# Kernel tuning notes

Hardware: AMD Instinct MI355X
Metric: run time of the kernel (lower is better)

The kernel has to match this reference:

```python
import jax, jax.numpy as jnp
import numpy as np

N = 50000      # number of graph nodes
D = 128        # in_dim == out_dim
R = 4          # num_ring
NNZ = 800000   # edges per ring (avg degree 16)


def setup_inputs() -> dict:
    key = jax.random.key(0)
    ks = jax.random.split(key, 12)
    s = 1.0 / np.sqrt(D)
    x = jax.random.normal(ks[0], (N, D), jnp.float32)
    W_self = jax.random.normal(ks[1], (D, D), jnp.float32) * s
    W_rings = jax.random.normal(ks[2], (R, D, D), jnp.float32) * s
    WC = jax.random.normal(ks[3], (D, D), jnp.float32) * s
    WD = jax.random.normal(ks[4], (D, D), jnp.float32) * s
    att_w = jax.random.normal(ks[5], (1, 2 * (R + 1) * D), jnp.float32) * s
    att_b = jnp.zeros((1,), jnp.float32)
    # degree^-0.5 style norms: positive, in (0, 1]
    out_deg_norm = jax.random.uniform(ks[6], (N, 1), jnp.float32, 0.05, 1.0)
    in_deg_norm = jax.random.uniform(ks[7], (N, 1), jnp.float32, 0.05, 1.0)
    rows = jax.random.randint(ks[8], (R, NNZ), 0, N, jnp.int32)
    cols = jax.random.randint(ks[9], (R, NNZ), 0, N, jnp.int32)
    return {"x": x, "W_self": W_self, "W_rings": W_rings, "WC": WC, "WD": WD,
            "att_w": att_w, "att_b": att_b, "out_deg_norm": out_deg_norm,
            "in_deg_norm": in_deg_norm, "rows": rows, "cols": cols}


def reference(x, W_self, W_rings, WC, WD, att_w, att_b, out_deg_norm, in_deg_norm, rows, cols):
    n, d = x.shape
    r = W_rings.shape[0]
    # ---- ring-wise sparse aggregation (dropout is identity at inference) ----
    z_self = x @ W_self.T                       # [N, D]
    z_list = [z_self]
    for i in range(r):
        h = (x @ W_rings[i].T) * out_deg_norm   # [N, D]
        # torch.sparse.mm(adj, h): out[row] += h[col] for each edge (row, col)
        z_i = jax.ops.segment_sum(h[cols[i]], rows[i], num_segments=n)
        z_list.append(z_i)
    z = jnp.concatenate(z_list, axis=1) * in_deg_norm   # [N, (R+1)*D]
    # ---- heterogeneous sensitivity interaction ----
    z3 = z.reshape(n, r + 1, d)                          # [N, R+1, D]
    z_hat_com = z3 @ WC                                  # [N, R+1, D]
    com_score = jnp.einsum('nrd,nsd->nrs', z_hat_com, z_hat_com)
    alpha_com = jax.nn.softmax(com_score, axis=-1)
    z_com = jnp.einsum('nrs,nsd->nrd', alpha_com, z_hat_com).reshape(n, -1)
    z_hat_dis = z3 @ WD                                  # [N, R+1, D]
    # pairwise differences: sub[n, r, s, :] = zd[n, r] - zd[n, s]
    sub = z_hat_dis[:, :, None, :] - z_hat_dis[:, None, :, :]   # [N, R+1, R+1, D]
    dis_score = jnp.einsum('nrd,nrsd->nrs', z_hat_dis, sub)
    alpha_dis = jax.nn.softmax(dis_score, axis=-1)
    z_dis = jnp.einsum('nrs,nrsd->nrd', alpha_dis, sub).reshape(n, -1)
    z_cat = jnp.concatenate([z_com, z_dis], axis=-1)     # [N, 2*(R+1)*D]
    beta = jax.nn.sigmoid(z_cat @ att_w.T + att_b)       # [N, 1]
    z_wave = beta * z_com + (1.0 - beta) * z_dis         # [N, (R+1)*D]
    return z_wave
```

## Files before the change

kernel.cpp:

```cpp
#include <hip/hip_runtime.h>
#include <hip/hip_bf16.h>

#define NN 50000
#define D 128
#define RR 4
#define NNZ 800000
#define NCHUNK 196

typedef float v2f    __attribute__((ext_vector_type(2)));
typedef float f32x4  __attribute__((ext_vector_type(4)));
typedef short bf16x8 __attribute__((ext_vector_type(8)));

static __device__ __forceinline__ unsigned short f2b(float f)
{
    __hip_bfloat16 h = __float2bfloat16(f);
    return *reinterpret_cast<unsigned short*>(&h);
}
static __device__ __forceinline__ float b2f(unsigned short u)
{
    union { unsigned u32; float f; } v; v.u32 = ((unsigned)u) << 16; return v.f;
}

__global__ __launch_bounds__(256) void hist_kernel(
    const int* __restrict__ rows, int* __restrict__ cnt)
{
    const int r = blockIdx.y;
    const int e = blockIdx.x * 256 + threadIdx.x;
    atomicAdd(&cnt[r * NN + rows[(size_t)r * NNZ + e]], 1);
}

__global__ __launch_bounds__(256) void scanA_kernel(
    const int* __restrict__ cnt, int* __restrict__ bsum)
{
    const int r = blockIdx.y, bx = blockIdx.x, t = threadIdx.x;
    const int idx = bx * 256 + t;
    int v = (idx < NN) ? cnt[r * NN + idx] : 0;
#pragma unroll
    for (int off = 32; off; off >>= 1) v += __shfl_xor(v, off);
    __shared__ int ws4[4];
    if ((t & 63) == 0) ws4[t >> 6] = v;
    __syncthreads();
    if (t == 0) bsum[r * NCHUNK + bx] = ws4[0] + ws4[1] + ws4[2] + ws4[3];
}

__global__ __launch_bounds__(256) void scanB_kernel(int* __restrict__ bsum)
{
    __shared__ int s[256];
    const int t = threadIdx.x;
    for (int r = 0; r < RR; ++r) {
        int v = (t < NCHUNK) ? bsum[r * NCHUNK + t] : 0;
        s[t] = v;
        __syncthreads();
        for (int off = 1; off < 256; off <<= 1) {
            int u = (t >= off) ? s[t - off] : 0;
            __syncthreads();
            s[t] += u;
            __syncthreads();
        }
        if (t < NCHUNK) bsum[r * NCHUNK + t] = s[t] - v;
        __syncthreads();
    }
}

__global__ __launch_bounds__(256) void scanC_kernel(
    const int* __restrict__ cnt, const int* __restrict__ bsum,
    int* __restrict__ rowptr, int* __restrict__ cursor)
{
    const int r = blockIdx.y, bx = blockIdx.x, t = threadIdx.x;
    const int idx = bx * 256 + t;
    int v = (idx < NN) ? cnt[r * NN + idx] : 0;
    __shared__ int s[256];
    s[t] = v;
    __syncthreads();
    for (int off = 1; off < 256; off <<= 1) {
        int u = (t >= off) ? s[t - off] : 0;
        __syncthreads();
        s[t] += u;
        __syncthreads();
    }
    const int excl = bsum[r * NCHUNK + bx] + s[t] - v;
    if (idx <= NN) rowptr[r * (NN + 1) + idx] = excl;
    if (idx < NN)  cursor[r * NN + idx] = excl;
}

__global__ __launch_bounds__(256) void fill_kernel(
    const int* __restrict__ rows, const int* __restrict__ cols,
    int* __restrict__ cursor, int* __restrict__ perm)
{
    const int r = blockIdx.y;
    const int e = blockIdx.x * 256 + threadIdx.x;
    const int row = rows[(size_t)r * NNZ + e];
    const int pos = atomicAdd(&cursor[r * NN + row], 1);
    perm[(size_t)r * NNZ + pos] = cols[(size_t)r * NNZ + e];
}

__global__ __launch_bounds__(256) void convw_kernel(
    const float* __restrict__ Wself, const float* __restrict__ Wrings,
    unsigned short* __restrict__ wh, unsigned short* __restrict__ wl)
{
    int idx = blockIdx.x * 256 + threadIdx.x;
    int jg = idx >> 7, k = idx & 127;
    float f = (jg < 128) ? Wself[(size_t)jg * 128 + k]
                         : Wrings[(size_t)(jg - 128) * 128 + k];
    unsigned short hi = f2b(f);
    wh[idx] = hi;
    wl[idx] = f2b(f - b2f(hi));
}

__global__ __launch_bounds__(256) void gemm_kernel(
    const float* __restrict__ x,
    const unsigned short* __restrict__ wh, const unsigned short* __restrict__ wl,
    const float* __restrict__ odn, float* __restrict__ out,
    float* __restrict__ h, int ct0, int nj, int ring0)
{
    const int t = threadIdx.x;
    const int w = t >> 6, l = t & 63;
    const int lr = l & 15, lk = l >> 4;
    const int n0 = blockIdx.x * 16;

    bf16x8 ah[4], al[4];
    const float* xr = x + (size_t)(n0 + lr) * D + lk * 8;
#pragma unroll
    for (int ks = 0; ks < 4; ++ks) {
        float4 v0 = *(const float4*)(xr + ks * 32);
        float4 v1 = *(const float4*)(xr + ks * 32 + 4);
        float f[8] = {v0.x, v0.y, v0.z, v0.w, v1.x, v1.y, v1.z, v1.w};
#pragma unroll
        for (int j = 0; j < 8; ++j) {
            unsigned short hi = f2b(f[j]);
            ah[ks][j] = (short)hi;
            al[ks][j] = (short)f2b(f[j] - b2f(hi));
        }
    }

    float od[4];
#pragma unroll
    for (int q = 0; q < 4; ++q) od[q] = odn[n0 + lk * 4 + q];

    for (int j = 0; j < nj; ++j) {
        const int ct = ct0 + w + 4 * j;
        const int colg = ct * 16 + lr;
        f32x4 acc = {0.f, 0.f, 0.f, 0.f};
#pragma unroll
        for (int ks = 0; ks < 4; ++ks) {
            bf16x8 bh = *(const bf16x8*)&wh[(size_t)colg * D + ks * 32 + lk * 8];
            bf16x8 bl = *(const bf16x8*)&wl[(size_t)colg * D + ks * 32 + lk * 8];
            acc = __builtin_amdgcn_mfma_f32_16x16x32_bf16(ah[ks], bh, acc, 0, 0, 0);
            acc = __builtin_amdgcn_mfma_f32_16x16x32_bf16(al[ks], bh, acc, 0, 0, 0);
            acc = __builtin_amdgcn_mfma_f32_16x16x32_bf16(ah[ks], bl, acc, 0, 0, 0);
        }
        if (ct < 8) {
#pragma unroll
            for (int q = 0; q < 4; ++q) {
                int n = n0 + lk * 4 + q;
                out[(size_t)n * 640 + colg] = acc[q];
            }
        } else {
            const int r = (ct >> 3) - 1 - ring0;
            const int d = (ct & 7) * 16 + lr;
#pragma unroll
            for (int q = 0; q < 4; ++q) {
                int n = n0 + lk * 4 + q;
                h[((size_t)r * NN + n) * D + d] = acc[q] * od[q];
            }
        }
    }
}

__global__ __launch_bounds__(256) void gather_kernel(
    const float* __restrict__ h, const int* __restrict__ rp,
    const int* __restrict__ pm, float* __restrict__ z, int csr_base)
{
    const int hr = blockIdx.y;
    const int cr = hr + csr_base;
    const int ln = threadIdx.x & 63;
    const int row = blockIdx.x * 4 + (threadIdx.x >> 6);
    const int* rpr = rp + (size_t)cr * (NN + 1);
    const int s = rpr[row], e = rpr[row + 1];
    const float* hb = h + (size_t)hr * NN * D;
    const int* pmr = pm + (size_t)cr * NNZ;

    float2 acc = make_float2(0.f, 0.f);
    int i = s;
    for (; i + 4 <= e; i += 4) {
        int c0 = pmr[i], c1 = pmr[i + 1], c2 = pmr[i + 2], c3 = pmr[i + 3];
        float2 v0 = *(const float2*)&hb[(size_t)c0 * D + ln * 2];
        float2 v1 = *(const float2*)&hb[(size_t)c1 * D + ln * 2];
        float2 v2 = *(const float2*)&hb[(size_t)c2 * D + ln * 2];
        float2 v3 = *(const float2*)&hb[(size_t)c3 * D + ln * 2];
        acc.x += v0.x + v1.x + v2.x + v3.x;
        acc.y += v0.y + v1.y + v2.y + v3.y;
    }
    for (; i < e; ++i) {
        float2 v = *(const float2*)&hb[(size_t)pmr[i] * D + ln * 2];
        acc.x += v.x; acc.y += v.y;
    }
    *(float2*)&z[(size_t)row * 640 + (cr + 1) * 128 + ln * 2] = acc;
}

__device__ __forceinline__ int sidx(int r, int s)
{
    if (r > s) { int t = r; r = s; s = t; }
    return r * 5 + s - (r * (r + 1)) / 2;
}

__global__ __launch_bounds__(1024, 4) void interact_kernel(
    float* __restrict__ z,
    const float* __restrict__ WC, const float* __restrict__ WD,
    const float* __restrict__ att_w, const float* __restrict__ att_b,
    const float* __restrict__ idn, int iters)
{
    __shared__ f32x4 WP[D * 64];
    const int t = threadIdx.x;
    for (int k = t; k < D * 64; k += 1024) {
        int d = k >> 6, l = k & 63;
        WP[k] = (f32x4){WC[d * 128 + l], WC[d * 128 + 64 + l],
                        WD[d * 128 + l], WD[d * 128 + 64 + l]};
    }
    __syncthreads();

    const int w  = t >> 6;
    const int ln = t & 63;
    const float ab = att_b[0];

    v2f awc[5], awd[5];
#pragma unroll
    for (int r = 0; r < 5; ++r) {
        awc[r] = (v2f){att_w[r * 128 + ln], att_w[r * 128 + 64 + ln]};
        awd[r] = (v2f){att_w[640 + r * 128 + ln], att_w[640 + r * 128 + 64 + ln]};
    }

    for (int it = 0; it < iters; ++it) {
        const int n = (it * gridDim.x + blockIdx.x) * 16 + w;
        if (n >= NN) break;
        const float nf = idn[n];
        const float* zn = z + (size_t)n * 640;

        v2f ac[5], ad[5];
#pragma unroll
        for (int r = 0; r < 5; ++r) { ac[r] = (v2f)0.f; ad[r] = (v2f)0.f; }
        for (int d0 = 0; d0 < D; d0 += 4) {
            float4 zr[5];
#pragma unroll
            for (int r = 0; r < 5; ++r) zr[r] = *(const float4*)(zn + r * 128 + d0);
#pragma unroll
            for (int dd = 0; dd < 4; ++dd) {
                f32x4 wp = WP[(d0 + dd) * 64 + ln];
                v2f wc = (v2f){wp.x, wp.y};
                v2f wd = (v2f){wp.z, wp.w};
#pragma unroll
                for (int r = 0; r < 5; ++r) {
                    float zv = (&zr[r].x)[dd];
                    ac[r] += wc * zv;
                    ad[r] += wd * zv;
                }
            }
        }
#pragma unroll
        for (int r = 0; r < 5; ++r) { ac[r] *= nf; ad[r] *= nf; }

        float pc[15], pd[15];
        {
            int k = 0;
#pragma unroll
            for (int r = 0; r < 5; ++r)
#pragma unroll
                for (int s = r; s < 5; ++s, ++k) {
                    v2f qc = ac[r] * ac[s];
                    v2f qd = ad[r] * ad[s];
                    float vc = qc.x + qc.y;
                    float vd = qd.x + qd.y;
#pragma unroll
                    for (int off = 32; off; off >>= 1) {
                        vc += __shfl_xor(vc, off);
                        vd += __shfl_xor(vd, off);
                    }
                    pc[k] = vc; pd[k] = vd;
                }
        }

        v2f zcom[5], zdis[5];
#pragma unroll
        for (int r = 0; r < 5; ++r) {
            float sc[5], m = -1e30f;
#pragma unroll
            for (int s = 0; s < 5; ++s) { sc[s] = pc[sidx(r, s)]; m = fmaxf(m, sc[s]); }
            float e[5], se = 0.f;
#pragma unroll
            for (int s = 0; s < 5; ++s) { e[s] = __expf(sc[s] - m); se += e[s]; }
            float inv = 1.f / se;
            v2f a2 = (v2f)0.f;
#pragma unroll
            for (int s = 0; s < 5; ++s) a2 += ac[s] * e[s];
            zcom[r] = a2 * inv;

            float q = pd[sidx(r, r)];
            float sd[5], md = -1e30f;
#pragma unroll
            for (int s = 0; s < 5; ++s) { sd[s] = q - pd[sidx(r, s)]; md = fmaxf(md, sd[s]); }
            float ed[5], sed = 0.f;
#pragma unroll
            for (int s = 0; s < 5; ++s) { ed[s] = __expf(sd[s] - md); sed += ed[s]; }
            float invd = 1.f / sed;
            v2f d2 = (v2f)0.f;
#pragma unroll
            for (int s = 0; s < 5; ++s) d2 += ad[s] * ed[s];
            zdis[r] = ad[r] - d2 * invd;
        }

        v2f p2 = (v2f)0.f;
#pragma unroll
        for (int r = 0; r < 5; ++r) p2 += awc[r] * zcom[r] + awd[r] * zdis[r];
        float part = p2.x + p2.y;
#pragma unroll
        for (int off = 32; off; off >>= 1) part += __shfl_xor(part, off);
        const float beta = 1.f / (1.f + __expf(-(part + ab)));
        const float omb  = 1.f - beta;

        float* zo = z + (size_t)n * 640;
#pragma unroll
        for (int r = 0; r < 5; ++r) {
            v2f o = zcom[r] * beta + zdis[r] * omb;
            zo[r * 128 + ln]      = o.x;
            zo[r * 128 + 64 + ln] = o.y;
        }
    }
}

extern "C" void kernel_launch(void* const* d_in, const int* in_sizes, int n_in,
                              void* d_out, int out_size, void* d_ws, size_t ws_size,
                              hipStream_t stream)
{
    const float* x      = (const float*)d_in[0];
    const float* W_self = (const float*)d_in[1];
    const float* W_ring = (const float*)d_in[2];
    const float* WC     = (const float*)d_in[3];
    const float* WD     = (const float*)d_in[4];
    const float* att_w  = (const float*)d_in[5];
    const float* att_b  = (const float*)d_in[6];
    const float* odn    = (const float*)d_in[7];
    const float* idn    = (const float*)d_in[8];
    const int*   rows   = (const int*)d_in[9];
    const int*   cols   = (const int*)d_in[10];
    float* out = (float*)d_out;

    const size_t wb_sz  = (size_t)640 * 128 * 2;
    const size_t h1_sz  = (size_t)NN * D * 4;
    const size_t cnt_sz = (size_t)RR * NN * 4;
    const size_t rp_sz  = (size_t)RR * (NN + 1) * 4;
    const size_t cur_sz = (size_t)RR * NN * 4;
    const size_t bs_sz  = 4096;
    const size_t pm_sz  = (size_t)RR * NNZ * 4;
    const size_t fixed  = 2 * wb_sz + cnt_sz + rp_sz + cur_sz + bs_sz + pm_sz;
    const bool big = ws_size >= fixed + RR * h1_sz + 4096;

    char* p = (char*)d_ws;
    unsigned short* wh = (unsigned short*)p; p += wb_sz;
    unsigned short* wl = (unsigned short*)p; p += wb_sz;
    float* h    = (float*)p; p += (big ? RR : 1) * h1_sz;
    int* cnt    = (int*)p; p += cnt_sz;
    int* rowptr = (int*)p; p += rp_sz;
    int* cursor = (int*)p; p += cur_sz;
    int* bsum   = (int*)p; p += bs_sz;
    int* perm   = (int*)p;

    convw_kernel<<<320, 256, 0, stream>>>(W_self, W_ring, wh, wl);

    hipMemsetAsync(cnt, 0, cnt_sz, stream);
    hist_kernel<<<dim3(NNZ / 256, RR), 256, 0, stream>>>(rows, cnt);
    scanA_kernel<<<dim3(NCHUNK, RR), 256, 0, stream>>>(cnt, bsum);
    scanB_kernel<<<1, 256, 0, stream>>>(bsum);
    scanC_kernel<<<dim3(NCHUNK, RR), 256, 0, stream>>>(cnt, bsum, rowptr, cursor);
    fill_kernel<<<dim3(NNZ / 256, RR), 256, 0, stream>>>(rows, cols, cursor, perm);

    if (big) {
        gemm_kernel<<<NN / 16, 256, 0, stream>>>(x, wh, wl, odn, out, h, 0, 10, 0);
        gather_kernel<<<dim3(NN / 4, RR), 256, 0, stream>>>(h, rowptr, perm, out, 0);
    } else {
        gemm_kernel<<<NN / 16, 256, 0, stream>>>(x, wh, wl, odn, out, h, 0, 2, 0);
        for (int r = 0; r < RR; ++r) {
            gemm_kernel<<<NN / 16, 256, 0, stream>>>(x, wh, wl, odn, out, h,
                                                     8 * (r + 1), 2, r);
            gather_kernel<<<dim3(NN / 4, 1), 256, 0, stream>>>(h, rowptr, perm, out, r);
        }
    }

    const int gridI = 256;
    const int iters = (NN + gridI * 16 - 1) / (gridI * 16);
    interact_kernel<<<gridI, 1024, 0, stream>>>(out, WC, WD, att_w, att_b, idn, iters);
}
```

Measured before the change: 1.221 ms.

## Compute interaction projections with split-bf16 MFMA and stage results in LDS

The interaction kernel's z@WC and z@WD projections move from scalar FP32 FMAs over an LDS-resident weight table to 3-pass split-bf16 MFMA, fed by transposed hi/lo bf16 weights from a new conversion kernel. Each 512-thread block handles 16 nodes: the MFMA outputs go to shared memory, then the softmax/attention stage reads them back per node. The goal is to take the dense projection cost off the vector ALUs. In exchange it uses about 80KB of LDS per block, which may limit occupancy, and the bf16 hi/lo split slightly changes numerics.

After: 1.158 ms. -5.2%, faster.

```diff
diff --git a/kernel.cpp b/kernel.cpp
--- a/kernel.cpp
+++ b/kernel.cpp
@@ -107,6 +107,22 @@
     wl[idx] = f2b(f - b2f(hi));
 }
 
+__global__ __launch_bounds__(256) void convt_kernel(
+    const float* __restrict__ WC, const float* __restrict__ WD,
+    unsigned short* __restrict__ wct_h, unsigned short* __restrict__ wct_l,
+    unsigned short* __restrict__ wdt_h, unsigned short* __restrict__ wdt_l)
+{
+    int idx = blockIdx.x * 256 + threadIdx.x;
+    int kk = idx >> 7, col = idx & 127;
+    float c = WC[idx];
+    float d = WD[idx];
+    unsigned short ch = f2b(c), dh = f2b(d);
+    wct_h[col * 128 + kk] = ch;
+    wct_l[col * 128 + kk] = f2b(c - b2f(ch));
+    wdt_h[col * 128 + kk] = dh;
+    wdt_l[col * 128 + kk] = f2b(d - b2f(dh));
+}
+
 __global__ __launch_bounds__(256) void gemm_kernel(
     const float* __restrict__ x,
     const unsigned short* __restrict__ wh, const unsigned short* __restrict__ wl,
@@ -143,11 +159,11 @@
         f32x4 acc = {0.f, 0.f, 0.f, 0.f};
 #pragma unroll
         for (int ks = 0; ks < 4; ++ks) {
-            bf16x8 bh = *(const bf16x8*)&wh[(size_t)colg * D + ks * 32 + lk * 8];
-            bf16x8 bl = *(const bf16x8*)&wl[(size_t)colg * D + ks * 32 + lk * 8];
-            acc = __builtin_amdgcn_mfma_f32_16x16x32_bf16(ah[ks], bh, acc, 0, 0, 0);
-            acc = __builtin_amdgcn_mfma_f32_16x16x32_bf16(al[ks], bh, acc, 0, 0, 0);
-            acc = __builtin_amdgcn_mfma_f32_16x16x32_bf16(ah[ks], bl, acc, 0, 0, 0);
+            bf16x8 bhv = *(const bf16x8*)&wh[(size_t)colg * D + ks * 32 + lk * 8];
+            bf16x8 blv = *(const bf16x8*)&wl[(size_t)colg * D + ks * 32 + lk * 8];
+            acc = __builtin_amdgcn_mfma_f32_16x16x32_bf16(ah[ks], bhv, acc, 0, 0, 0);
+            acc = __builtin_amdgcn_mfma_f32_16x16x32_bf16(al[ks], bhv, acc, 0, 0, 0);
+            acc = __builtin_amdgcn_mfma_f32_16x16x32_bf16(ah[ks], blv, acc, 0, 0, 0);
         }
         if (ct < 8) {
 #pragma unroll
@@ -204,60 +220,89 @@
     return r * 5 + s - (r * (r + 1)) / 2;
 }
 
-__global__ __launch_bounds__(1024, 4) void interact_kernel(
+__global__ __launch_bounds__(512, 4) void interact2_kernel(
     float* __restrict__ z,
-    const float* __restrict__ WC, const float* __restrict__ WD,
+    const unsigned short* __restrict__ wct_h, const unsigned short* __restrict__ wct_l,
+    const unsigned short* __restrict__ wdt_h, const unsigned short* __restrict__ wdt_l,
     const float* __restrict__ att_w, const float* __restrict__ att_b,
-    const float* __restrict__ idn, int iters)
-{
-    __shared__ f32x4 WP[D * 64];
-    const int t = threadIdx.x;
-    for (int k = t; k < D * 64; k += 1024) {
-        int d = k >> 6, l = k & 63;
-        WP[k] = (f32x4){WC[d * 128 + l], WC[d * 128 + 64 + l],
-                        WD[d * 128 + l], WD[d * 128 + 64 + l]};
-    }
+    const float* __restrict__ idn)
+{
+    __shared__ float SB[2 * 5 * 16 * 128];
+
+    const int t  = threadIdx.x;
+    const int w  = t >> 6;
+    const int l  = t & 63;
+    const int lr = l & 15;
+    const int lk = l >> 4;
+    const int n0 = blockIdx.x * 16;
+
+    const int mm = w >> 2;
+    const int nq = w & 3;
+    const unsigned short* bhp = mm ? wdt_h : wct_h;
+    const unsigned short* blp = mm ? wdt_l : wct_l;
+
+    f32x4 acc[5][2];
+#pragma unroll
+    for (int mt = 0; mt < 5; ++mt) {
+        acc[mt][0] = (f32x4){0.f, 0.f, 0.f, 0.f};
+        acc[mt][1] = (f32x4){0.f, 0.f, 0.f, 0.f};
+    }
+
+#pragma unroll
+    for (int mt = 0; mt < 5; ++mt) {
+        bf16x8 ah[4], al[4];
+        const float* ap = z + (size_t)(n0 + lr) * 640 + mt * 128 + lk * 8;
+#pragma unroll
+        for (int ks = 0; ks < 4; ++ks) {
+            float4 v0 = *(const float4*)(ap + ks * 32);
+            float4 v1 = *(const float4*)(ap + ks * 32 + 4);
+            float f[8] = {v0.x, v0.y, v0.z, v0.w, v1.x, v1.y, v1.z, v1.w};
+#pragma unroll
+            for (int j = 0; j < 8; ++j) {
+                unsigned short hi = f2b(f[j]);
+                ah[ks][j] = (short)hi;
+                al[ks][j] = (short)f2b(f[j] - b2f(hi));
+            }
+        }
+#pragma unroll
+        for (int nt = 0; nt < 2; ++nt) {
+            const int col = nq * 32 + nt * 16 + lr;
+#pragma unroll
+            for (int ks = 0; ks < 4; ++ks) {
+                bf16x8 vh = *(const bf16x8*)&bhp[(size_t)col * 128 + ks * 32 + lk * 8];
+                bf16x8 vl = *(const bf16x8*)&blp[(size_t)col * 128 + ks * 32 + lk * 8];
+                acc[mt][nt] = __builtin_amdgcn_mfma_f32_16x16x32_bf16(ah[ks], vh, acc[mt][nt], 0, 0, 0);
+                acc[mt][nt] = __builtin_amdgcn_mfma_f32_16x16x32_bf16(al[ks], vh, acc[mt][nt], 0, 0, 0);
+                acc[mt][nt] = __builtin_amdgcn_mfma_f32_16x16x32_bf16(ah[ks], vl, acc[mt][nt], 0, 0, 0);
+            }
+        }
+    }
+
+#pragma unroll
+    for (int mt = 0; mt < 5; ++mt)
+#pragma unroll
+        for (int nt = 0; nt < 2; ++nt) {
+            const int col = nq * 32 + nt * 16 + lr;
+#pragma unroll
+            for (int q = 0; q < 4; ++q) {
+                const int nd = lk * 4 + q;
+                SB[(((mm * 5 + mt) * 16) + nd) * 128 + col] = acc[mt][nt][q];
+            }
+        }
     __syncthreads();
 
-    const int w  = t >> 6;
-    const int ln = t & 63;
-    const float ab = att_b[0];
-
-    v2f awc[5], awd[5];
-#pragma unroll
-    for (int r = 0; r < 5; ++r) {
-        awc[r] = (v2f){att_w[r * 128 + ln], att_w[r * 128 + 64 + ln]};
-        awd[r] = (v2f){att_w[640 + r * 128 + ln], att_w[640 + r * 128 + 64 + ln]};
-    }
-
-    for (int it = 0; it < iters; ++it) {
-        const int n = (it * gridDim.x + blockIdx.x) * 16 + w;
-        if (n >= NN) break;
+#pragma unroll
+    for (int ii = 0; ii < 2; ++ii) {
+        const int nd = w + ii * 8;
+        const int n  = n0 + nd;
         const float nf = idn[n];
-        const float* zn = z + (size_t)n * 640;
-
-        v2f ac[5], ad[5];
-#pragma unroll
-        for (int r = 0; r < 5; ++r) { ac[r] = (v2f)0.f; ad[r] = (v2f)0.f; }
-        for (int d0 = 0; d0 < D; d0 += 4) {
-            float4 zr[5];
-#pragma unroll
-            for (int r = 0; r < 5; ++r) zr[r] = *(const float4*)(zn + r * 128 + d0);
-#pragma unroll
-            for (int dd = 0; dd < 4; ++dd) {
-                f32x4 wp = WP[(d0 + dd) * 64 + ln];
-                v2f wc = (v2f){wp.x, wp.y};
-                v2f wd = (v2f){wp.z, wp.w};
-#pragma unroll
-                for (int r = 0; r < 5; ++r) {
-                    float zv = (&zr[r].x)[dd];
-                    ac[r] += wc * zv;
-                    ad[r] += wd * zv;
-                }
-            }
-        }
-#pragma unroll
-        for (int r = 0; r < 5; ++r) { ac[r] *= nf; ad[r] *= nf; }
+
+        v2f ar[5], dr[5];
+#pragma unroll
+        for (int r = 0; r < 5; ++r) {
+            ar[r] = *(const v2f*)&SB[((r * 16) + nd) * 128 + 2 * l] * nf;
+            dr[r] = *(const v2f*)&SB[(((5 + r) * 16) + nd) * 128 + 2 * l] * nf;
+        }
 
         float pc[15], pd[15];
         {
@@ -266,8 +311,8 @@
             for (int r = 0; r < 5; ++r)
 #pragma unroll
                 for (int s = r; s < 5; ++s, ++k) {
-                    v2f qc = ac[r] * ac[s];
-                    v2f qd = ad[r] * ad[s];
+                    v2f qc = ar[r] * ar[s];
+                    v2f qd = dr[r] * dr[s];
                     float vc = qc.x + qc.y;
                     float vd = qd.x + qd.y;
 #pragma unroll
@@ -291,38 +336,39 @@
             float inv = 1.f / se;
             v2f a2 = (v2f)0.f;
 #pragma unroll
-            for (int s = 0; s < 5; ++s) a2 += ac[s] * e[s];
+            for (int s = 0; s < 5; ++s) a2 += ar[s] * e[s];
             zcom[r] = a2 * inv;
 
-            float q = pd[sidx(r, r)];
+            float qq = pd[sidx(r, r)];
             float sd[5], md = -1e30f;
 #pragma unroll
-            for (int s = 0; s < 5; ++s) { sd[s] = q - pd[sidx(r, s)]; md = fmaxf(md, sd[s]); }
+            for (int s = 0; s < 5; ++s) { sd[s] = qq - pd[sidx(r, s)]; md = fmaxf(md, sd[s]); }
             float ed[5], sed = 0.f;
 #pragma unroll
             for (int s = 0; s < 5; ++s) { ed[s] = __expf(sd[s] - md); sed += ed[s]; }
             float invd = 1.f / sed;
             v2f d2 = (v2f)0.f;
 #pragma unroll
-            for (int s = 0; s < 5; ++s) d2 += ad[s] * ed[s];
-            zdis[r] = ad[r] - d2 * invd;
+            for (int s = 0; s < 5; ++s) d2 += dr[s] * ed[s];
+            zdis[r] = dr[r] - d2 * invd;
         }
 
         v2f p2 = (v2f)0.f;
 #pragma unroll
-        for (int r = 0; r < 5; ++r) p2 += awc[r] * zcom[r] + awd[r] * zdis[r];
+        for (int r = 0; r < 5; ++r) {
+            p2 += (*(const v2f*)&att_w[r * 128 + 2 * l]) * zcom[r];
+            p2 += (*(const v2f*)&att_w[640 + r * 128 + 2 * l]) * zdis[r];
+        }
         float part = p2.x + p2.y;
 #pragma unroll
         for (int off = 32; off; off >>= 1) part += __shfl_xor(part, off);
-        const float beta = 1.f / (1.f + __expf(-(part + ab)));
+        const float beta = 1.f / (1.f + __expf(-(part + att_b[0])));
         const float omb  = 1.f - beta;
 
-        float* zo = z + (size_t)n * 640;
 #pragma unroll
         for (int r = 0; r < 5; ++r) {
             v2f o = zcom[r] * beta + zdis[r] * omb;
-            zo[r * 128 + ln]      = o.x;
-            zo[r * 128 + 64 + ln] = o.y;
+            *(v2f*)&z[(size_t)n * 640 + r * 128 + 2 * l] = o;
         }
     }
 }
@@ -345,18 +391,23 @@
     float* out = (float*)d_out;
 
     const size_t wb_sz  = (size_t)640 * 128 * 2;
+    const size_t wt_sz  = (size_t)128 * 128 * 2;
     const size_t h1_sz  = (size_t)NN * D * 4;
     const size_t cnt_sz = (size_t)RR * NN * 4;
     const size_t rp_sz  = (size_t)RR * (NN + 1) * 4;
     const size_t cur_sz = (size_t)RR * NN * 4;
     const size_t bs_sz  = 4096;
     const size_t pm_sz  = (size_t)RR * NNZ * 4;
-    const size_t fixed  = 2 * wb_sz + cnt_sz + rp_sz + cur_sz + bs_sz + pm_sz;
+    const size_t fixed  = 2 * wb_sz + 4 * wt_sz + cnt_sz + rp_sz + cur_sz + bs_sz + pm_sz;
     const bool big = ws_size >= fixed + RR * h1_sz + 4096;
 
     char* p = (char*)d_ws;
-    unsigned short* wh = (unsigned short*)p; p += wb_sz;
-    unsigned short* wl = (unsigned short*)p; p += wb_sz;
+    unsigned short* wh    = (unsigned short*)p; p += wb_sz;
+    unsigned short* wl    = (unsigned short*)p; p += wb_sz;
+    unsigned short* wct_h = (unsigned short*)p; p += wt_sz;
+    unsigned short* wct_l = (unsigned short*)p; p += wt_sz;
+    unsigned short* wdt_h = (unsigned short*)p; p += wt_sz;
+    unsigned short* wdt_l = (unsigned short*)p; p += wt_sz;
     float* h    = (float*)p; p += (big ? RR : 1) * h1_sz;
     int* cnt    = (int*)p; p += cnt_sz;
     int* rowptr = (int*)p; p += rp_sz;
@@ -365,6 +416,7 @@
     int* perm   = (int*)p;
 
     convw_kernel<<<320, 256, 0, stream>>>(W_self, W_ring, wh, wl);
+    convt_kernel<<<64, 256, 0, stream>>>(WC, WD, wct_h, wct_l, wdt_h, wdt_l);
 
     hipMemsetAsync(cnt, 0, cnt_sz, stream);
     hist_kernel<<<dim3(NNZ / 256, RR), 256, 0, stream>>>(rows, cnt);
@@ -385,7 +437,6 @@
         }
     }
 
-    const int gridI = 256;
-    const int iters = (NN + gridI * 16 - 1) / (gridI * 16);
-    interact_kernel<<<gridI, 1024, 0, stream>>>(out, WC, WD, att_w, att_b, idn, iters);
-}
+    interact2_kernel<<<NN / 16, 512, 0, stream>>>(out, wct_h, wct_l, wdt_h, wdt_l,
+                                                  att_w, att_b, idn);
+}
```
